# Kernel optimization log

Hardware: AMD Instinct MI355X
Metric: run time of the kernel (lower is better)

Reference implementation:

```python
import jax, jax.numpy as jnp
import numpy as np

N, C, EMB, OUT, HID, HEADS, K, R, E = 100000, 256, 256, 8, 256, 4, 20000, 16, 800000
RETR_IN = EMB + OUT + 1  # z_retr + o_retr + retr_score
DH = HID // HEADS


def _lin(key, fi, fo):
    return jax.random.normal(key, (fi, fo), jnp.float32) / np.sqrt(fi)


def setup_inputs() -> dict:
    key = jax.random.key(0)
    ks = jax.random.split(key, 32)
    inp = {
        "h_cone": jax.random.normal(ks[0], (N, C), jnp.float32),
        "z_retr": jax.random.normal(ks[1], (K, R, EMB), jnp.float32),
        "o_retr": jax.random.normal(ks[2], (K, R, OUT), jnp.float32),
        "retr_score": jax.random.uniform(ks[3], (K, R), jnp.float32),
        "teacher_yhat": jax.random.normal(ks[4], (N, OUT), jnp.float32),
        "outpin_nids": jax.random.randint(ks[5], (K,), 0, N, jnp.int32),
        "edge_index": jax.random.randint(ks[6], (2, E), 0, N, jnp.int32),
        # retr_proj: Linear(RETR_IN,HID) -> ReLU -> Linear(HID,HID)
        "rp_W1": _lin(ks[7], RETR_IN, HID), "rp_b1": jnp.zeros((HID,), jnp.float32),
        "rp_W2": _lin(ks[8], HID, HID),     "rp_b2": jnp.zeros((HID,), jnp.float32),
        # query_proj: Linear(C, HID)
        "qp_W": _lin(ks[9], C, HID), "qp_b": jnp.zeros((HID,), jnp.float32),
        # MultiheadAttention packed q/k/v projection + output projection
        "in_proj_W": _lin(ks[10], HID, 3 * HID), "in_proj_b": jnp.zeros((3 * HID,), jnp.float32),
        "out_proj_W": _lin(ks[11], HID, HID),    "out_proj_b": jnp.zeros((HID,), jnp.float32),
        # gate_net: Linear(C+HID,HID) -> ReLU -> Linear(HID,C) -> Sigmoid
        "gate_W1": _lin(ks[12], C + HID, HID), "gate_b1": jnp.zeros((HID,), jnp.float32),
        "gate_W2": _lin(ks[13], HID, C),       "gate_b2": jnp.zeros((C,), jnp.float32),
        # update_net: Linear(HID,C) -> ReLU -> Linear(C,C)
        "upd_W1": _lin(ks[14], HID, C), "upd_b1": jnp.zeros((C,), jnp.float32),
        "upd_W2": _lin(ks[15], C, C),   "upd_b2": jnp.zeros((C,), jnp.float32),
        # cone GNN (LocalGNN gcn, 2 layers): C->HID, HID->HID with sym-normalized aggregation
        "gnn_W1": _lin(ks[16], C, HID),   "gnn_b1": jnp.zeros((HID,), jnp.float32),
        "gnn_W2": _lin(ks[17], HID, HID), "gnn_b2": jnp.zeros((HID,), jnp.float32),
        # head: Linear(HID,HID) -> ReLU -> Linear(HID,OUT) (orig zero-init; random here for nontrivial grads)
        "head_W1": _lin(ks[18], HID, HID), "head_b1": jnp.zeros((HID,), jnp.float32),
        "head_W2": _lin(ks[19], HID, OUT) * 0.01, "head_b2": jnp.zeros((OUT,), jnp.float32),
    }
    return inp


def _forward(h_cone, z_retr, o_retr, retr_score, teacher_yhat, outpin_nids, edge_index,
             rp_W1, rp_b1, rp_W2, rp_b2, qp_W, qp_b, in_proj_W, in_proj_b,
             out_proj_W, out_proj_b, gate_W1, gate_b1, gate_W2, gate_b2,
             upd_W1, upd_b1, upd_W2, upd_b2, gnn_W1, gnn_b1, gnn_W2, gnn_b2,
             head_W1, head_b1, head_W2, head_b2):
    # ---- retrieval aggregation: per-outpin cross-attn over R neighbors ----
    kv_in = jnp.concatenate([z_retr, o_retr, retr_score[..., None]], axis=-1)  # [K,R,RETR_IN]
    kv = jax.nn.relu(kv_in @ rp_W1 + rp_b1) @ rp_W2 + rp_b2                    # [K,R,HID]
    hq = h_cone[outpin_nids]                                                   # [K,C] gather
    q = hq @ qp_W + qp_b                                                       # [K,HID]
    Wq, Wk, Wv = jnp.split(in_proj_W, 3, axis=1)
    bq, bk, bv = jnp.split(in_proj_b, 3)
    qh = (q @ Wq + bq).reshape(K, HEADS, DH)
    kh = (kv @ Wk + bk).reshape(K, R, HEADS, DH)
    vh = (kv @ Wv + bv).reshape(K, R, HEADS, DH)
    att = jax.nn.softmax(jnp.einsum('khd,krhd->khr', qh, kh) / np.sqrt(DH), axis=-1)
    ctx = jnp.einsum('khr,krhd->khd', att, vh).reshape(K, HID)
    retr_ctx = ctx @ out_proj_W + out_proj_b                                   # [K,HID]
    # ---- gated outpin fusion + scatter back ----
    gate = jax.nn.sigmoid(jax.nn.relu(jnp.concatenate([hq, retr_ctx], axis=-1) @ gate_W1 + gate_b1) @ gate_W2 + gate_b2)
    update = jax.nn.relu(retr_ctx @ upd_W1 + upd_b1) @ upd_W2 + upd_b2         # [K,C]
    h = h_cone.at[outpin_nids].set(hq + gate * update)                         # scatter
    # ---- cone GNN: 2-layer GCN with self loops, symmetric normalization ----
    loops = jnp.arange(N, dtype=edge_index.dtype)
    src = jnp.concatenate([edge_index[0], loops])
    dst = jnp.concatenate([edge_index[1], loops])
    deg = jax.ops.segment_sum(jnp.ones_like(src, jnp.float32), dst, num_segments=N)
    norm = (jax.lax.rsqrt(deg[src]) * jax.lax.rsqrt(deg[dst]))[:, None]
    x1 = h @ gnn_W1 + gnn_b1
    h1 = jax.nn.relu(jax.ops.segment_sum(x1[src] * norm, dst, num_segments=N))
    x2 = h1 @ gnn_W2 + gnn_b2
    h2 = jax.ops.segment_sum(x2[src] * norm, dst, num_segments=N)
    # ---- residual head ----
    delta = jax.nn.relu(h2 @ head_W1 + head_b1) @ head_W2 + head_b2
    return teacher_yhat + delta


def reference(h_cone, z_retr, o_retr, retr_score, teacher_yhat, outpin_nids, edge_index,
              rp_W1, rp_b1, rp_W2, rp_b2, qp_W, qp_b, in_proj_W, in_proj_b,
              out_proj_W, out_proj_b, gate_W1, gate_b1, gate_W2, gate_b2,
              upd_W1, upd_b1, upd_W2, upd_b2, gnn_W1, gnn_b1, gnn_W2, gnn_b2,
              head_W1, head_b1, head_W2, head_b2):
    return _forward(h_cone, z_retr, o_retr, retr_score, teacher_yhat, outpin_nids, edge_index,
                    rp_W1, rp_b1, rp_W2, rp_b2, qp_W, qp_b, in_proj_W, in_proj_b,
                    out_proj_W, out_proj_b, gate_W1, gate_b1, gate_W2, gate_b2,
                    upd_W1, upd_b1, upd_W2, upd_b2, gnn_W1, gnn_b1, gnn_W2, gnn_b2,
                    head_W1, head_b1, head_W2, head_b2)
```

## Files before the change

### kernel.cpp

```cpp
#include <hip/hip_runtime.h>
#include <cstdint>
#include <cstddef>

typedef unsigned short u16;

#define NN    100000
#define OUTD  8
#define KKP   20000
#define RR    16
#define EE    800000
#define KRR   (KKP*RR)
#define KP    20096
#define NP    100096

typedef __bf16 v8bf __attribute__((ext_vector_type(8)));
typedef float  v4f  __attribute__((ext_vector_type(4)));

__device__ __forceinline__ float b2f(u16 u) {
    union { uint32_t i; float f; } v; v.i = (uint32_t)u << 16; return v.f;
}
__device__ __forceinline__ u16 f2b(float f) {
    union { float f; uint32_t i; } v; v.f = f;
    uint32_t i = v.i;
    return (u16)((i + 0x7fffu + ((i >> 16) & 1u)) >> 16);
}
__device__ __forceinline__ uint32_t pk2(float a, float b) {
    return (uint32_t)f2b(a) | ((uint32_t)f2b(b) << 16);
}

#define GLDS(g, l) __builtin_amdgcn_global_load_lds(                         \
    (const __attribute__((address_space(1))) void*)(g),                      \
    (__attribute__((address_space(3))) void*)(l), 16, 0, 0)

#define WAITVL(n) asm volatile("s_waitcnt vmcnt(" #n ") lgkmcnt(0)" ::: "memory")
#define BAR() __builtin_amdgcn_s_barrier()

template <int EPI, int OMODE, int A32, int RETR>
__launch_bounds__(256)
__global__ void gemm_bf_k(const void* __restrict__ Av, int lda, int M, int Ka,
                          const u16* __restrict__ Wt,
                          const float* __restrict__ bias,
                          void* __restrict__ Cv, int ldc,
                          const float* __restrict__ o_ex,
                          const float* __restrict__ s_ex,
                          const float* __restrict__ Wex)
{
    constexpr int NBA = A32 ? 2 : 3;
    __shared__ u16 As[NBA * 128 * 32];
    __shared__ u16 Bs[3 * 128 * 32];
    const int row0 = blockIdx.x * 128;
    const int col0 = blockIdx.y * 128;
    const int t    = threadIdx.x;
    const int lane = t & 63;
    const int w    = t >> 6;
    const int wm   = w & 1, wn = w >> 1;

    const int idx0 = t, idx1 = t + 256;
    const u16* Ab = (const u16*)Av;
    const float* Af = (const float*)Av;
    const u16* Ag0 = Ab + (size_t)(row0 + (idx0 >> 2)) * lda + (idx0 & 3) * 8;
    const u16* Ag1 = Ab + (size_t)(row0 + (idx1 >> 2)) * lda + (idx1 & 3) * 8;
    const float* Af0 = Af + (size_t)(row0 + (idx0 >> 2)) * lda + (idx0 & 3) * 8;
    const float* Af1 = Af + (size_t)(row0 + (idx1 >> 2)) * lda + (idx1 & 3) * 8;
    const u16* Bg0 = Wt + (size_t)(col0 + (idx0 >> 2)) * Ka + (idx0 & 3) * 8;
    const u16* Bg1 = Wt + (size_t)(col0 + (idx1 >> 2)) * Ka + (idx1 & 3) * 8;
    const int s0 = idx0 * 8, s1 = idx1 * 8;

    auto stageB = [&](int bi, int kk) {
        u16* bp = Bs + bi * (128 * 32);
        GLDS(Bg0 + kk, bp + s0);
        GLDS(Bg1 + kk, bp + s1);
    };
    auto stageA = [&](int bi, int kk) {
        u16* ap = As + bi * (128 * 32);
        GLDS(Ag0 + kk, ap + s0);
        GLDS(Ag1 + kk, ap + s1);
    };

    float4 P0, P1, P2, P3, Q0, Q1, Q2, Q3;
    auto loadP = [&](int kk) {
        P0 = *(const float4*)(Af0 + kk);     P1 = *(const float4*)(Af0 + kk + 4);
        P2 = *(const float4*)(Af1 + kk);     P3 = *(const float4*)(Af1 + kk + 4);
    };
    auto loadQ = [&](int kk) {
        Q0 = *(const float4*)(Af0 + kk);     Q1 = *(const float4*)(Af0 + kk + 4);
        Q2 = *(const float4*)(Af1 + kk);     Q3 = *(const float4*)(Af1 + kk + 4);
    };
    auto writeP = [&](int bi) {
        u16* ap = As + bi * (128 * 32);
        uint4 u0, u1;
        u0.x = pk2(P0.x, P0.y); u0.y = pk2(P0.z, P0.w);
        u0.z = pk2(P1.x, P1.y); u0.w = pk2(P1.z, P1.w);
        u1.x = pk2(P2.x, P2.y); u1.y = pk2(P2.z, P2.w);
        u1.z = pk2(P3.x, P3.y); u1.w = pk2(P3.z, P3.w);
        *(uint4*)(ap + s0) = u0;
        *(uint4*)(ap + s1) = u1;
    };
    auto writeQ = [&](int bi) {
        u16* ap = As + bi * (128 * 32);
        uint4 u0, u1;
        u0.x = pk2(Q0.x, Q0.y); u0.y = pk2(Q0.z, Q0.w);
        u0.z = pk2(Q1.x, Q1.y); u0.w = pk2(Q1.z, Q1.w);
        u1.x = pk2(Q2.x, Q2.y); u1.y = pk2(Q2.z, Q2.w);
        u1.z = pk2(Q3.x, Q3.y); u1.w = pk2(Q3.z, Q3.w);
        *(uint4*)(ap + s0) = u0;
        *(uint4*)(ap + s1) = u1;
    };

    v4f acc[4][4];
#pragma unroll
    for (int mi = 0; mi < 4; mi++)
#pragma unroll
        for (int ni = 0; ni < 4; ni++) acc[mi][ni] = 0.f;

    const int fr = lane & 15;
    const int fq = (lane >> 4) * 8;
    const int nk = Ka >> 5;

    if (A32) {
        loadP(0);
        stageB(0, 0);
        if (nk > 1) {
            loadQ(32);
            stageB(1, 32);
        }
        writeP(0);
        if (nk > 1) { WAITVL(6); }
        else        { WAITVL(0); }
    } else {
        stageA(0, 0); stageB(0, 0);
        if (nk > 1) { stageA(1, 32); stageB(1, 32); WAITVL(4); }
        else        { WAITVL(0); }
    }
    BAR();

    int rb = 0, sb = 2;
    for (int tI = 0; tI < nk; ++tI) {
        const bool st = (tI + 2) < nk;
        const int kk2 = (tI + 2) << 5;
        if (st) {
            if (A32) {
                if (tI & 1) loadQ(kk2); else loadP(kk2);
                stageB(sb, kk2);
            } else {
                stageA(sb, kk2);
                stageB(sb, kk2);
            }
        }
        const u16* Ar = As + (A32 ? (tI & 1) : rb) * (128 * 32);
        const u16* Br = Bs + rb * (128 * 32);
        v8bf af[4], bv[4];
#pragma unroll
        for (int mi = 0; mi < 4; mi++)
            af[mi] = *(const v8bf*)&Ar[(wm * 64 + mi * 16 + fr) * 32 + fq];
#pragma unroll
        for (int ni = 0; ni < 4; ni++)
            bv[ni] = *(const v8bf*)&Br[(wn * 64 + ni * 16 + fr) * 32 + fq];
#pragma unroll
        for (int mi = 0; mi < 4; mi++)
#pragma unroll
            for (int ni = 0; ni < 4; ni++)
                acc[mi][ni] = __builtin_amdgcn_mfma_f32_16x16x32_bf16(
                    af[mi], bv[ni], acc[mi][ni], 0, 0, 0);

        if (tI + 1 < nk) {
            if (A32) {
                if (tI & 1) writeP((tI + 1) & 1); else writeQ((tI + 1) & 1);
            }
            if (st) { if (A32) { WAITVL(6); } else { WAITVL(4); } }
            else    { WAITVL(0); }
            BAR();
        }
        rb = (rb == 2) ? 0 : rb + 1;
        sb = (sb == 2) ? 0 : sb + 1;
    }

    const int crow = wm * 64 + (lane >> 4) * 4;
    const int ccol = wn * 64 + (lane & 15);
    float bias_v[4];
#pragma unroll
    for (int ni = 0; ni < 4; ni++) bias_v[ni] = bias[col0 + ccol + ni * 16];

    u16*   Cb = (u16*)Cv;
    float* Cf = (float*)Cv;
#pragma unroll
    for (int mi = 0; mi < 4; mi++) {
#pragma unroll
        for (int reg = 0; reg < 4; reg++) {
            int r = row0 + crow + mi * 16 + reg;
            if (r >= M) continue;
            float ov[8], sv;
            if (RETR) {
#pragma unroll
                for (int u = 0; u < 8; u++) ov[u] = o_ex[(size_t)r * 8 + u];
                sv = s_ex[r];
            }
#pragma unroll
            for (int ni = 0; ni < 4; ni++) {
                int c = col0 + ccol + ni * 16;
                float v = acc[mi][ni][reg] + bias_v[ni];
                if (RETR) {
                    float e = sv * Wex[8 * 256 + c];
#pragma unroll
                    for (int u = 0; u < 8; u++) e = fmaf(ov[u], Wex[u * 256 + c], e);
                    v += e;
                }
                if (EPI == 1) v = fmaxf(v, 0.f);
                if (EPI == 2) v = 1.f / (1.f + expf(-v));
                if (OMODE == 1) Cb[(size_t)r * ldc + c] = f2b(v);
                else            Cf[(size_t)r * ldc + c] = v;
            }
        }
    }
}

__global__ void wtpose_k(const float* __restrict__ W, int ld, int coloff,
                         int fi, int Kpad, u16* __restrict__ Wt)
{
    int g = blockIdx.x * 256 + threadIdx.x;
    if (g >= 256 * Kpad) return;
    int o = g / Kpad, i = g - o * Kpad;
    Wt[g] = f2b(i < fi ? W[(size_t)i * ld + coloff + o] : 0.f);
}

__global__ void wfuse_k(const float* __restrict__ A, const float* __restrict__ Binw,
                        int ldb, int off, const float* __restrict__ ba,
                        const float* __restrict__ bb,
                        u16* __restrict__ Wt_out, float* __restrict__ bias_out)
{
    __shared__ float As[256];
    __shared__ float bs[256];
    int i = blockIdx.x, j = threadIdx.x;
    As[j] = A[(size_t)i * 256 + j];
    bs[j] = ba[j];
    __syncthreads();
    float acc = 0.f, accb = 0.f;
    for (int m = 0; m < 256; m++) {
        float bv = Binw[(size_t)m * ldb + off + j];
        acc = fmaf(As[m], bv, acc);
        if (i == 0) accb = fmaf(bs[m], bv, accb);
    }
    Wt_out[(size_t)j * 256 + i] = f2b(acc);
    if (i == 0) bias_out[j] = bb[j] + accb;
}

__global__ void conv_f2b_k(const float* __restrict__ src, u16* __restrict__ dst, size_t n4)
{
    size_t g = (size_t)blockIdx.x * 256 + threadIdx.x;
    if (g >= n4) return;
    float4 v = ((const float4*)src)[g];
    ((ushort4*)dst)[g] = make_ushort4(f2b(v.x), f2b(v.y), f2b(v.z), f2b(v.w));
}

__global__ void gather_hq_k(const float* __restrict__ hc, const int* __restrict__ nids,
                            u16* __restrict__ acat)
{
    int t = threadIdx.x;
    int k = blockIdx.x * 4 + (t >> 6);
    int c = t & 63;
    if (k >= KKP) return;
    int nid = nids[k];
    float4 v = ((const float4*)hc)[(size_t)nid * 64 + c];
    *(ushort4*)&acat[(size_t)k * 512 + c * 4] =
        make_ushort4(f2b(v.x), f2b(v.y), f2b(v.z), f2b(v.w));
}

__launch_bounds__(256)
__global__ void att_fused_k(const u16* __restrict__ qh, const u16* __restrict__ khv,
                            u16* __restrict__ ctx)
{
    int k = blockIdx.x;
    int t = threadIdx.x;
    int lane = t & 63;
    float qv = b2f(qh[(size_t)k * 256 + t]);
    const u16* kp = khv + (size_t)k * (RR * 512) + t;
    const u16* vp = kp + 256;
    float myscore = -1e30f;
#pragma unroll
    for (int r = 0; r < RR; r++) {
        float p = qv * b2f(kp[r * 512]);
#pragma unroll
        for (int off = 1; off < 64; off <<= 1) p += __shfl_xor(p, off);
        if (lane == r) myscore = p * 0.125f;
    }
    float m = (lane < RR) ? myscore : -1e30f;
#pragma unroll
    for (int off = 1; off < 16; off <<= 1) m = fmaxf(m, __shfl_xor(m, off));
    float pe = (lane < RR) ? expf(myscore - m) : 0.f;
    float ssum = pe;
#pragma unroll
    for (int off = 1; off < 16; off <<= 1) ssum += __shfl_xor(ssum, off);
    float pn = pe / ssum;
    float acc = 0.f;
#pragma unroll
    for (int r = 0; r < RR; r++) {
        float ar = __shfl(pn, r);
        acc = fmaf(ar, b2f(vp[r * 512]), acc);
    }
    ctx[(size_t)k * 256 + t] = f2b(acc);
}

__global__ void winner_k(const int* __restrict__ nids, int* __restrict__ winner)
{
    int gid = blockIdx.x * 256 + threadIdx.x;
    if (gid < KKP) atomicMax(&winner[nids[gid]], gid);
}

__global__ void scatter_h_k(const int* __restrict__ nids, const int* __restrict__ winner,
                            const float* __restrict__ hc, const float* __restrict__ gate,
                            const float* __restrict__ upd, u16* __restrict__ hb)
{
    int t = threadIdx.x;
    int k = blockIdx.x * 4 + (t >> 6);
    int c = t & 63;
    if (k >= KKP) return;
    int nid = nids[k];
    if (winner[nid] != k) return;
    float4 hv = ((const float4*)hc)[(size_t)nid * 64 + c];
    float4 gv = ((const float4*)gate)[(size_t)k * 64 + c];
    float4 uv = ((const float4*)upd)[(size_t)k * 64 + c];
    *(ushort4*)&hb[(size_t)nid * 256 + c * 4] = make_ushort4(
        f2b(hv.x + gv.x * uv.x), f2b(hv.y + gv.y * uv.y),
        f2b(hv.z + gv.z * uv.z), f2b(hv.w + gv.w * uv.w));
}

__global__ void edge_count_k(const int* __restrict__ dst, int* __restrict__ cnt, int e)
{
    int gid = blockIdx.x * 256 + threadIdx.x;
    if (gid < e) atomicAdd(&cnt[dst[gid]], 1);
}

__global__ void isd_k(const int* __restrict__ cnt, float* __restrict__ isd, int n)
{
    int gid = blockIdx.x * 256 + threadIdx.x;
    if (gid < n) isd[gid] = rsqrtf((float)(cnt[gid] + 1));
}

#define SCANB 1024
__global__ void scan1_k(const int* __restrict__ in, int* __restrict__ out,
                        int* __restrict__ bsums, int n)
{
    __shared__ int s[SCANB];
    int tid = threadIdx.x;
    int gid = blockIdx.x * SCANB + tid;
    int v = (gid < n) ? in[gid] : 0;
    s[tid] = v;
    __syncthreads();
    for (int off = 1; off < SCANB; off <<= 1) {
        int add = (tid >= off) ? s[tid - off] : 0;
        __syncthreads();
        s[tid] += add;
        __syncthreads();
    }
    if (gid < n) out[gid] = s[tid] - v;
    if (tid == SCANB - 1) bsums[blockIdx.x] = s[tid];
}

__global__ void scan2_k(int* bsums, int nb)
{
    if (threadIdx.x == 0 && blockIdx.x == 0) {
        int run = 0;
        for (int i = 0; i < nb; i++) { int v = bsums[i]; bsums[i] = run; run += v; }
    }
}

__global__ void scan3_k(int* __restrict__ out, const int* __restrict__ bsums, int n, int total)
{
    int gid = blockIdx.x * SCANB + threadIdx.x;
    if (gid < n) out[gid] += bsums[blockIdx.x];
    if (gid == 0) out[n] = total;
}

__global__ void csr_scatter_k(const int* __restrict__ src, const int* __restrict__ dst,
                              const int* __restrict__ row_start, int* __restrict__ cursor,
                              const float* __restrict__ isd,
                              int* __restrict__ csr_src, float* __restrict__ csr_w, int e)
{
    int gid = blockIdx.x * 256 + threadIdx.x;
    if (gid < e) {
        int sP = src[gid], dP = dst[gid];
        int pos = row_start[dP] + atomicAdd(&cursor[dP], 1);
        csr_src[pos] = sP;
        csr_w[pos] = isd[sP] * isd[dP];
    }
}

template <int RELU>
__launch_bounds__(256)
__global__ void gnn_agg_k(const u16* __restrict__ x, const int* __restrict__ row_start,
                          const int* __restrict__ csr_src, const float* __restrict__ csr_w,
                          const float* __restrict__ isd, u16* __restrict__ outp)
{
    int node = blockIdx.x * 4 + (threadIdx.x >> 6);
    int lane = threadIdx.x & 63;
    if (node >= NN) return;
    float si = isd[node];
    float sii = si * si;
    ushort4 sv = ((const ushort4*)x)[(size_t)node * 64 + lane];
    float a0 = b2f(sv.x) * sii, a1 = b2f(sv.y) * sii;
    float a2 = b2f(sv.z) * sii, a3 = b2f(sv.w) * sii;
    int s0 = row_start[node], s1 = row_start[node + 1];
    for (int j = s0; j < s1; j++) {
        int sP = csr_src[j];
        float wv = csr_w[j];
        ushort4 v = ((const ushort4*)x)[(size_t)sP * 64 + lane];
        a0 = fmaf(b2f(v.x), wv, a0);
        a1 = fmaf(b2f(v.y), wv, a1);
        a2 = fmaf(b2f(v.z), wv, a2);
        a3 = fmaf(b2f(v.w), wv, a3);
    }
    if (RELU) {
        a0 = fmaxf(a0, 0.f); a1 = fmaxf(a1, 0.f);
        a2 = fmaxf(a2, 0.f); a3 = fmaxf(a3, 0.f);
    }
    ((ushort4*)outp)[(size_t)node * 64 + lane] =
        make_ushort4(f2b(a0), f2b(a1), f2b(a2), f2b(a3));
}

__launch_bounds__(256)
__global__ void head_out_k(const u16* __restrict__ thid, const float* __restrict__ W2,
                           const float* __restrict__ b2, const float* __restrict__ teacher,
                           float* __restrict__ outp, int n)
{
    __shared__ float ts[32][257];
    __shared__ float w2s[256 * 8];
    int t = threadIdx.x;
    int rbase = blockIdx.x * 32;
    for (int i = t; i < 2048; i += 256) w2s[i] = W2[i];
    for (int i = t; i < 32 * 256; i += 256) {
        int rr = i >> 8, cc = i & 255;
        int gr = rbase + rr;
        ts[rr][cc] = (gr < n) ? b2f(thid[(size_t)gr * 256 + cc]) : 0.f;
    }
    __syncthreads();
    int rr = t >> 3, cc = t & 7;
    int gr = rbase + rr;
    if (gr >= n) return;
    float acc = b2[cc];
    for (int kk = 0; kk < 256; kk++)
        acc = fmaf(ts[rr][kk], w2s[kk * 8 + cc], acc);
    outp[(size_t)gr * 8 + cc] = teacher[(size_t)gr * 8 + cc] + acc;
}

extern "C" void kernel_launch(void* const* d_in, const int* in_sizes, int n_in,
                              void* d_out, int out_size, void* d_ws, size_t ws_size,
                              hipStream_t stream)
{
    (void)in_sizes; (void)n_in; (void)out_size; (void)ws_size;
    const float* h_cone     = (const float*)d_in[0];
    const float* z_retr     = (const float*)d_in[1];
    const float* o_retr     = (const float*)d_in[2];
    const float* retr_score = (const float*)d_in[3];
    const float* teacher    = (const float*)d_in[4];
    const int*   nids       = (const int*)d_in[5];
    const int*   edge       = (const int*)d_in[6];
    const float* rp_W1 = (const float*)d_in[7];   const float* rp_b1 = (const float*)d_in[8];
    const float* rp_W2 = (const float*)d_in[9];   const float* rp_b2 = (const float*)d_in[10];
    const float* qp_W  = (const float*)d_in[11];  const float* qp_b  = (const float*)d_in[12];
    const float* inW   = (const float*)d_in[13];  const float* inB   = (const float*)d_in[14];
    const float* outW  = (const float*)d_in[15];  const float* outB  = (const float*)d_in[16];
    const float* gW1   = (const float*)d_in[17];  const float* gB1   = (const float*)d_in[18];
    const float* gW2   = (const float*)d_in[19];  const float* gB2   = (const float*)d_in[20];
    const float* uW1   = (const float*)d_in[21];  const float* uB1   = (const float*)d_in[22];
    const float* uW2   = (const float*)d_in[23];  const float* uB2   = (const float*)d_in[24];
    const float* gnW1  = (const float*)d_in[25];  const float* gnB1  = (const float*)d_in[26];
    const float* gnW2  = (const float*)d_in[27];  const float* gnB2  = (const float*)d_in[28];
    const float* hW1   = (const float*)d_in[29];  const float* hB1   = (const float*)d_in[30];
    const float* hW2   = (const float*)d_in[31];  const float* hB2   = (const float*)d_in[32];
    float* out = (float*)d_out;

    char* ws = (char*)d_ws;
    size_t off = 0;
    auto alloc = [&](size_t bytes) -> void* {
        void* p = ws + off;
        off = (off + bytes + 255) & ~(size_t)255;
        return p;
    };
    u16* hidden = (u16*)alloc((size_t)KRR * 256 * 2);
    u16* khv    = (u16*)alloc((size_t)KRR * 512 * 2);
    u16* qhb    = (u16*)alloc((size_t)KP * 256 * 2);
    u16* ctxb   = (u16*)alloc((size_t)KP * 256 * 2);
    u16* acat   = (u16*)alloc((size_t)KP * 512 * 2);
    u16* ghid   = (u16*)alloc((size_t)KP * 256 * 2);
    float* gate = (float*)alloc((size_t)KP * 256 * 4);
    u16* uhid   = (u16*)alloc((size_t)KP * 256 * 2);
    float* upd  = (float*)alloc((size_t)KP * 256 * 4);
    u16* wt_rp1 = (u16*)alloc(256 * 256 * 2);
    u16* wt_kv  = (u16*)alloc(512 * 256 * 2);
    u16* wt_qf  = (u16*)alloc(256 * 256 * 2);
    u16* wt_o   = (u16*)alloc(256 * 256 * 2);
    u16* wt_g1  = (u16*)alloc(256 * 512 * 2);
    u16* wt_g2  = (u16*)alloc(256 * 256 * 2);
    u16* wt_u1  = (u16*)alloc(256 * 256 * 2);
    u16* wt_u2  = (u16*)alloc(256 * 256 * 2);
    u16* wt_gn1 = (u16*)alloc(256 * 256 * 2);
    u16* wt_gn2 = (u16*)alloc(256 * 256 * 2);
    u16* wt_h1  = (u16*)alloc(256 * 256 * 2);
    float* bias_kv = (float*)alloc(512 * 4);
    float* bias_qf = (float*)alloc(256 * 4);
    int*   winner    = (int*)alloc(NN * 4);
    int*   cnt       = (int*)alloc(NN * 4);
    int*   cursor    = (int*)alloc(NN * 4);
    int*   row_start = (int*)alloc((NN + 1) * 4);
    int*   bsums     = (int*)alloc(1024 * 4);
    float* isd       = (float*)alloc(NN * 4);
    int*   csr_src   = (int*)alloc((size_t)EE * 4);
    float* csr_w     = (float*)alloc((size_t)EE * 4);

    const size_t NPE = (size_t)NP * 256;
    u16* gZ0 = hidden;
    u16* gZ1 = hidden + NPE;
    u16* gZ2 = hidden + 2 * NPE;

    const int* esrc = edge;
    const int* edst = edge + EE;

    auto wtp = [&](const float* W, int ld, int coloff, int fi, int Kpad, u16* Wt) {
        wtpose_k<<<(256 * Kpad + 255) / 256, 256, 0, stream>>>(W, ld, coloff, fi, Kpad, Wt);
    };

    hipMemsetAsync(cnt, 0, NN * 4, stream);
    hipMemsetAsync(cursor, 0, NN * 4, stream);
    edge_count_k<<<(EE + 255) / 256, 256, 0, stream>>>(edst, cnt, EE);
    isd_k<<<(NN + 255) / 256, 256, 0, stream>>>(cnt, isd, NN);
    int nb = (NN + SCANB - 1) / SCANB;
    scan1_k<<<nb, SCANB, 0, stream>>>(cnt, row_start, bsums, NN);
    scan2_k<<<1, 64, 0, stream>>>(bsums, nb);
    scan3_k<<<nb, SCANB, 0, stream>>>(row_start, bsums, NN, EE);
    csr_scatter_k<<<(EE + 255) / 256, 256, 0, stream>>>(esrc, edst, row_start, cursor, isd,
                                                        csr_src, csr_w, EE);

    wtp(rp_W1, 256, 0, 256, 256, wt_rp1);
    wfuse_k<<<256, 256, 0, stream>>>(rp_W2, inW, 768, 256, rp_b2, inB + 256, wt_kv, bias_kv);
    wfuse_k<<<256, 256, 0, stream>>>(rp_W2, inW, 768, 512, rp_b2, inB + 512,
                                     wt_kv + 256 * 256, bias_kv + 256);
    wfuse_k<<<256, 256, 0, stream>>>(qp_W, inW, 768, 0, qp_b, inB, wt_qf, bias_qf);
    wtp(outW, 256, 0, 256, 256, wt_o);
    wtp(gW1,  256, 0, 512, 512, wt_g1);
    wtp(gW2,  256, 0, 256, 256, wt_g2);
    wtp(uW1,  256, 0, 256, 256, wt_u1);
    wtp(uW2,  256, 0, 256, 256, wt_u2);
    wtp(gnW1, 256, 0, 256, 256, wt_gn1);
    wtp(gnW2, 256, 0, 256, 256, wt_gn2);
    wtp(hW1,  256, 0, 256, 256, wt_h1);
    gather_hq_k<<<(KKP + 3) / 4, 256, 0, stream>>>(h_cone, nids, acat);

    gemm_bf_k<1, 1, 1, 1><<<dim3(KRR / 128, 2), 256, 0, stream>>>(
        z_retr, 256, KRR, 256, wt_rp1, rp_b1, hidden, 256,
        o_retr, retr_score, rp_W1 + 256 * 256);
    gemm_bf_k<0, 1, 0, 0><<<dim3(KRR / 128, 4), 256, 0, stream>>>(
        hidden, 256, KRR, 256, wt_kv, bias_kv, khv, 512, nullptr, nullptr, nullptr);
    gemm_bf_k<0, 1, 0, 0><<<dim3((KKP + 127) / 128, 2), 256, 0, stream>>>(
        acat, 512, KKP, 256, wt_qf, bias_qf, qhb, 256, nullptr, nullptr, nullptr);

    att_fused_k<<<KKP, 256, 0, stream>>>(qhb, khv, ctxb);
    gemm_bf_k<0, 1, 0, 0><<<dim3((KKP + 127) / 128, 2), 256, 0, stream>>>(
        ctxb, 256, KKP, 256, wt_o, outB, acat + 256, 512, nullptr, nullptr, nullptr);

    gemm_bf_k<1, 1, 0, 0><<<dim3((KKP + 127) / 128, 2), 256, 0, stream>>>(
        acat, 512, KKP, 512, wt_g1, gB1, ghid, 256, nullptr, nullptr, nullptr);
    gemm_bf_k<2, 2, 0, 0><<<dim3((KKP + 127) / 128, 2), 256, 0, stream>>>(
        ghid, 256, KKP, 256, wt_g2, gB2, gate, 256, nullptr, nullptr, nullptr);
    gemm_bf_k<1, 1, 0, 0><<<dim3((KKP + 127) / 128, 2), 256, 0, stream>>>(
        acat + 256, 512, KKP, 256, wt_u1, uB1, uhid, 256, nullptr, nullptr, nullptr);
    gemm_bf_k<0, 2, 0, 0><<<dim3((KKP + 127) / 128, 2), 256, 0, stream>>>(
        uhid, 256, KKP, 256, wt_u2, uB2, upd, 256, nullptr, nullptr, nullptr);

    conv_f2b_k<<<(int)(((size_t)NN * 64 + 255) / 256), 256, 0, stream>>>(
        h_cone, gZ0, (size_t)NN * 64);
    hipMemsetAsync(winner, 0xFF, NN * 4, stream);
    winner_k<<<(KKP + 255) / 256, 256, 0, stream>>>(nids, winner);
    scatter_h_k<<<(KKP + 3) / 4, 256, 0, stream>>>(nids, winner, h_cone, gate, upd, gZ0);

    gemm_bf_k<0, 1, 0, 0><<<dim3((NN + 127) / 128, 2), 256, 0, stream>>>(
        gZ0, 256, NN, 256, wt_gn1, gnB1, gZ1, 256, nullptr, nullptr, nullptr);
    gnn_agg_k<1><<<(NN + 3) / 4, 256, 0, stream>>>(gZ1, row_start, csr_src, csr_w, isd, gZ2);
    gemm_bf_k<0, 1, 0, 0><<<dim3((NN + 127) / 128, 2), 256, 0, stream>>>(
        gZ2, 256, NN, 256, wt_gn2, gnB2, gZ0, 256, nullptr, nullptr, nullptr);
    gnn_agg_k<0><<<(NN + 3) / 4, 256, 0, stream>>>(gZ0, row_start, csr_src, csr_w, isd, gZ1);
    gemm_bf_k<1, 1, 0, 0><<<dim3((NN + 127) / 128, 2), 256, 0, stream>>>(
        gZ1, 256, NN, 256, wt_h1, hB1, gZ2, 256, nullptr, nullptr, nullptr);
    head_out_k<<<(NN + 31) / 32, 256, 0, stream>>>(gZ2, hW2, hB2, teacher, out, NN);
}
```

Before: 1.812 ms.

## Fuse retrieval MLP, attention scores and value projection into one kernel

Replaces the separate retr_proj GEMM, K/V GEMM, Q GEMM and attention kernel with a single per-128-row kernel. The hidden activations stay in shared memory and are never written to HBM. Attention scores use a precomputed per-query vector (Q times W_k folded per head), and V is projected on the fly and reduced with the softmax weights. This removes the large KRR x 512 khv buffer and its global-memory round-trips. In exchange the kernel is heavy: about 160KB of LDS with launch_bounds(256,1), so occupancy is low, and the precision of the key projection changes.

```diff
diff --git a/kernel.cpp b/kernel.cpp
--- a/kernel.cpp
+++ b/kernel.cpp
@@ -214,6 +214,238 @@
     }
 }
 
+__launch_bounds__(256, 1)
+__global__ void retrfuse_k(const float* __restrict__ Zf,
+                           const u16*  __restrict__ W1t,
+                           const float* __restrict__ b1,
+                           const float* __restrict__ o_ex,
+                           const float* __restrict__ s_ex,
+                           const u16*  __restrict__ wqk,
+                           const u16*  __restrict__ Wv,
+                           const float* __restrict__ bv2,
+                           u16* __restrict__ ctx)
+{
+    __shared__ __align__(16) u16 Az[128 * 256];
+    __shared__ __align__(16) u16 Ax[128 * 32];
+    __shared__ __align__(16) u16 Bp[2 * 128 * 32];
+    __shared__ __align__(16) u16 Hs[128 * 256];
+
+    float* attL = (float*)Bp;
+
+    const int bx = blockIdx.x;
+    const int row0 = bx * 128;
+    const int t = threadIdx.x, lane = t & 63, w = t >> 6;
+    const int wm = w & 1, wn = w >> 1;
+    const int fr = lane & 15, fq = (lane >> 4) * 8;
+    const int idx0 = t, idx1 = t + 256;
+
+    auto stageBt = [&](int tts) {
+        int p2 = (tts >= 9) ? 1 : 0;
+        int s2 = tts - p2 * 9;
+        const u16* g0 = W1t + (size_t)(p2 * 128 + (idx0 >> 2)) * 288 + (idx0 & 3) * 8 + s2 * 32;
+        const u16* g1 = W1t + (size_t)(p2 * 128 + (idx1 >> 2)) * 288 + (idx1 & 3) * 8 + s2 * 32;
+        u16* bp = Bp + (tts & 1) * (128 * 32);
+        GLDS(g0, bp + idx0 * 8);
+        GLDS(g1, bp + idx1 * 8);
+    };
+
+    {
+        const float* zb = Zf + (size_t)row0 * 256;
+        float4 pa[4], pb[4];
+#pragma unroll
+        for (int j = 0; j < 4; j++) {
+            int c = j * 256 + t, r = c >> 5, sl = c & 31;
+            const float* g = zb + (size_t)r * 256 + sl * 8;
+            pa[j] = *(const float4*)g;
+            pb[j] = *(const float4*)(g + 4);
+        }
+        stageBt(0);
+#pragma unroll
+        for (int j = 0; j < 16; j++) {
+            int c = j * 256 + t, r = c >> 5, sl = c & 31;
+            int jr = j & 3;
+            uint4 u;
+            u.x = pk2(pa[jr].x, pa[jr].y); u.y = pk2(pa[jr].z, pa[jr].w);
+            u.z = pk2(pb[jr].x, pb[jr].y); u.w = pk2(pb[jr].z, pb[jr].w);
+            *(uint4*)((char*)Az + (size_t)r * 512 + ((sl ^ (r & 7)) * 16)) = u;
+            int jn = j + 4;
+            if (jn < 16) {
+                int cn = jn * 256 + t, rn = cn >> 5, sn = cn & 31;
+                const float* gn = zb + (size_t)rn * 256 + sn * 8;
+                pa[jr] = *(const float4*)gn;
+                pb[jr] = *(const float4*)(gn + 4);
+            }
+        }
+#pragma unroll
+        for (int j = 0; j < 2; j++) {
+            int c = j * 256 + t, r = c >> 2, sl = c & 3;
+            int rg = row0 + r;
+            uint4 u = make_uint4(0u, 0u, 0u, 0u);
+            if (sl == 0) {
+                float4 o0 = *(const float4*)(o_ex + (size_t)rg * 8);
+                float4 o1 = *(const float4*)(o_ex + (size_t)rg * 8 + 4);
+                u.x = pk2(o0.x, o0.y); u.y = pk2(o0.z, o0.w);
+                u.z = pk2(o1.x, o1.y); u.w = pk2(o1.z, o1.w);
+            } else if (sl == 1) {
+                u.x = pk2(s_ex[rg], 0.f);
+            }
+            *(uint4*)((char*)Ax + r * 64 + ((sl ^ (r & 3)) * 16)) = u;
+        }
+        WAITVL(0);
+        BAR();
+    }
+
+    v4f acc[4][4];
+#pragma unroll
+    for (int mi = 0; mi < 4; mi++)
+#pragma unroll
+        for (int ni = 0; ni < 4; ni++) acc[mi][ni] = 0.f;
+
+    for (int tt = 0; tt < 18; ++tt) {
+        if (tt + 1 < 18) stageBt(tt + 1);
+        const int pass = (tt >= 9) ? 1 : 0;
+        const int s = tt - pass * 9;
+        const u16* Br = Bp + (tt & 1) * (128 * 32);
+        v8bf af[4], bb[4];
+#pragma unroll
+        for (int mi = 0; mi < 4; mi++) {
+            int row = wm * 64 + mi * 16 + fr;
+            if (s < 8)
+                af[mi] = *(const v8bf*)((const char*)Az + (size_t)row * 512 +
+                                        (((s * 4 + (fq >> 3)) ^ (row & 7)) * 16));
+            else
+                af[mi] = *(const v8bf*)((const char*)Ax + row * 64 +
+                                        (((fq >> 3) ^ (row & 3)) * 16));
+        }
+#pragma unroll
+        for (int ni = 0; ni < 4; ni++)
+            bb[ni] = *(const v8bf*)&Br[(wn * 64 + ni * 16 + fr) * 32 + fq];
+#pragma unroll
+        for (int mi = 0; mi < 4; mi++)
+#pragma unroll
+            for (int ni = 0; ni < 4; ni++)
+                acc[mi][ni] = __builtin_amdgcn_mfma_f32_16x16x32_bf16(
+                    af[mi], bb[ni], acc[mi][ni], 0, 0, 0);
+
+        if (s == 8) {
+            const int col0p = pass * 128;
+            const int crow = wm * 64 + (lane >> 4) * 4;
+            const int ccol = wn * 64 + fr;
+            float bvv[4];
+#pragma unroll
+            for (int ni = 0; ni < 4; ni++) bvv[ni] = b1[col0p + ccol + ni * 16];
+#pragma unroll
+            for (int mi = 0; mi < 4; mi++)
+#pragma unroll
+                for (int reg = 0; reg < 4; reg++) {
+                    int rl = crow + mi * 16 + reg;
+#pragma unroll
+                    for (int ni = 0; ni < 4; ni++) {
+                        int c = col0p + ccol + ni * 16;
+                        float v = fmaxf(acc[mi][ni][reg] + bvv[ni], 0.f);
+                        *(u16*)((char*)Hs + (size_t)rl * 512 +
+                                (((c >> 3) ^ (rl & 7)) * 16) + (c & 7) * 2) = f2b(v);
+                    }
+                }
+#pragma unroll
+            for (int mi = 0; mi < 4; mi++)
+#pragma unroll
+                for (int ni = 0; ni < 4; ni++) acc[mi][ni] = 0.f;
+        }
+        if (tt < 17) { WAITVL(0); BAR(); }
+    }
+
+    auto stageV = [&](int rr) {
+#pragma unroll
+        for (int j = 0; j < 4; j++) {
+            int c = j * 256 + t;
+            int tile = c >> 9, cc = c & 511;
+            int vr = cc >> 5, sp = cc & 31;
+            int nts = tile * 8 + rr;
+            const u16* g = Wv + (size_t)(nts * 16 + vr) * 256 + ((sp ^ (vr & 7)) * 8);
+            GLDS(g, (u16*)((char*)Az + 16384 + (tile * 2 + (rr & 1)) * 8192 + cc * 16));
+        }
+    };
+#pragma unroll
+    for (int j = 0; j < 4; j++) {
+        int c = j * 256 + t;
+        GLDS(wqk + (size_t)(bx * 8) * 1024 + c * 8, (u16*)((char*)Az + c * 16));
+    }
+    stageV(0);
+    WAITVL(4);
+    BAR();
+
+#pragma unroll
+    for (int kk = 0; kk < 2; kk++) {
+        int kloc = w * 2 + kk;
+        v4f sc; sc = 0.f;
+#pragma unroll
+        for (int s = 0; s < 8; s++) {
+            int row = kloc * 16 + fr;
+            v8bf ha = *(const v8bf*)((const char*)Hs + (size_t)row * 512 +
+                                     (((s * 4 + (fq >> 3)) ^ (row & 7)) * 16));
+            v4f zf; zf = 0.f;
+            v8bf bq = __builtin_bit_cast(v8bf, zf);
+            if (fr < 4)
+                bq = *(const v8bf*)((const char*)Az + kloc * 2048 + fr * 512 + s * 64 + fq * 2);
+            sc = __builtin_amdgcn_mfma_f32_16x16x32_bf16(ha, bq, sc, 0, 0, 0);
+        }
+        float s0 = sc[0] * 0.125f, s1 = sc[1] * 0.125f;
+        float s2 = sc[2] * 0.125f, s3 = sc[3] * 0.125f;
+        float mx = fmaxf(fmaxf(s0, s1), fmaxf(s2, s3));
+        mx = fmaxf(mx, __shfl_xor(mx, 16));
+        mx = fmaxf(mx, __shfl_xor(mx, 32));
+        float p0 = __expf(s0 - mx), p1 = __expf(s1 - mx);
+        float p2 = __expf(s2 - mx), p3 = __expf(s3 - mx);
+        float sm = p0 + p1 + p2 + p3;
+        sm += __shfl_xor(sm, 16);
+        sm += __shfl_xor(sm, 32);
+        float inv = 1.f / sm;
+        if (fr < 4) {
+            float4 a4 = make_float4(p0 * inv, p1 * inv, p2 * inv, p3 * inv);
+            *(float4*)&attL[kloc * 64 + fr * 16 + (lane >> 4) * 4] = a4;
+        }
+    }
+    WAITVL(0);
+    BAR();
+
+    const int khalf = w & 1, nth = w >> 1;
+    v8bf af4[4][8];
+#pragma unroll
+    for (int kj = 0; kj < 4; kj++) {
+        int row = (khalf * 4 + kj) * 16 + fr;
+#pragma unroll
+        for (int s = 0; s < 8; s++)
+            af4[kj][s] = *(const v8bf*)((const char*)Hs + (size_t)row * 512 +
+                                        (((s * 4 + (fq >> 3)) ^ (row & 7)) * 16));
+    }
+    for (int r = 0; r < 8; ++r) {
+        if (r < 7) stageV(r + 1);
+        int nt = nth * 8 + r;
+        const char* cb = (const char*)Az + 16384 + (nth * 2 + (r & 1)) * 8192;
+        v8bf bvf[8];
+#pragma unroll
+        for (int s = 0; s < 8; s++)
+            bvf[s] = *(const v8bf*)(cb + fr * 512 + (((s * 4 + (fq >> 3)) ^ (fr & 7)) * 16));
+        float bvb = bv2[nt * 16 + fr];
+#pragma unroll
+        for (int kj = 0; kj < 4; kj++) {
+            int kloc = khalf * 4 + kj;
+            v4f d; d = 0.f;
+#pragma unroll
+            for (int s = 0; s < 8; s++)
+                d = __builtin_amdgcn_mfma_f32_16x16x32_bf16(af4[kj][s], bvf[s], d, 0, 0, 0);
+            float4 av = *(const float4*)&attL[kloc * 64 + (nt >> 2) * 16 + (lane >> 4) * 4];
+            float val = av.x * d[0] + av.y * d[1] + av.z * d[2] + av.w * d[3];
+            val += __shfl_xor(val, 16);
+            val += __shfl_xor(val, 32);
+            if (lane < 16)
+                ctx[(size_t)(bx * 8 + kloc) * 256 + nt * 16 + lane] = f2b(val + bvb);
+        }
+        if (r < 7) { WAITVL(4); BAR(); }
+    }
+}
+
 __global__ void wtpose_k(const float* __restrict__ W, int ld, int coloff,
                          int fi, int Kpad, u16* __restrict__ Wt)
 {
@@ -226,7 +458,8 @@
 __global__ void wfuse_k(const float* __restrict__ A, const float* __restrict__ Binw,
                         int ldb, int off, const float* __restrict__ ba,
                         const float* __restrict__ bb,
-                        u16* __restrict__ Wt_out, float* __restrict__ bias_out)
+                        u16* __restrict__ Wt_out, float* __restrict__ bias_out,
+                        float* __restrict__ out32)
 {
     __shared__ float As[256];
     __shared__ float bs[256];
@@ -241,7 +474,33 @@
         if (i == 0) accb = fmaf(bs[m], bv, accb);
     }
     Wt_out[(size_t)j * 256 + i] = f2b(acc);
+    if (out32) out32[(size_t)j * 256 + i] = acc;
     if (i == 0) bias_out[j] = bb[j] + accb;
+}
+
+__global__ void qkfuse_k(const float* __restrict__ Qf32, const float* __restrict__ Wk32,
+                         const float* __restrict__ bqf,
+                         u16* __restrict__ Wtqk, float* __restrict__ bqk)
+{
+    __shared__ float wk[64];
+    __shared__ float bq[64];
+    int b = blockIdx.x;
+    int h = b >> 8, m = b & 255;
+    int c = threadIdx.x;
+    if (c < 64) {
+        wk[c] = Wk32[(size_t)(h * 64 + c) * 256 + m];
+        bq[c] = bqf[h * 64 + c];
+    }
+    __syncthreads();
+    float acc = 0.f;
+    for (int d = 0; d < 64; d++)
+        acc = fmaf(Qf32[(size_t)(h * 64 + d) * 256 + c], wk[d], acc);
+    Wtqk[(size_t)b * 256 + c] = f2b(acc);
+    if (c == 0) {
+        float ab = 0.f;
+        for (int d = 0; d < 64; d++) ab = fmaf(bq[d], wk[d], ab);
+        bqk[b] = ab;
+    }
 }
 
 __global__ void conv_f2b_k(const float* __restrict__ src, u16* __restrict__ dst, size_t n4)
@@ -263,41 +522,6 @@
     float4 v = ((const float4*)hc)[(size_t)nid * 64 + c];
     *(ushort4*)&acat[(size_t)k * 512 + c * 4] =
         make_ushort4(f2b(v.x), f2b(v.y), f2b(v.z), f2b(v.w));
-}
-
-__launch_bounds__(256)
-__global__ void att_fused_k(const u16* __restrict__ qh, const u16* __restrict__ khv,
-                            u16* __restrict__ ctx)
-{
-    int k = blockIdx.x;
-    int t = threadIdx.x;
-    int lane = t & 63;
-    float qv = b2f(qh[(size_t)k * 256 + t]);
-    const u16* kp = khv + (size_t)k * (RR * 512) + t;
-    const u16* vp = kp + 256;
-    float myscore = -1e30f;
-#pragma unroll
-    for (int r = 0; r < RR; r++) {
-        float p = qv * b2f(kp[r * 512]);
-#pragma unroll
-        for (int off = 1; off < 64; off <<= 1) p += __shfl_xor(p, off);
-        if (lane == r) myscore = p * 0.125f;
-    }
-    float m = (lane < RR) ? myscore : -1e30f;
-#pragma unroll
-    for (int off = 1; off < 16; off <<= 1) m = fmaxf(m, __shfl_xor(m, off));
-    float pe = (lane < RR) ? expf(myscore - m) : 0.f;
-    float ssum = pe;
-#pragma unroll
-    for (int off = 1; off < 16; off <<= 1) ssum += __shfl_xor(ssum, off);
-    float pn = pe / ssum;
-    float acc = 0.f;
-#pragma unroll
-    for (int r = 0; r < RR; r++) {
-        float ar = __shfl(pn, r);
-        acc = fmaf(ar, b2f(vp[r * 512]), acc);
-    }
-    ctx[(size_t)k * 256 + t] = f2b(acc);
 }
 
 __global__ void winner_k(const int* __restrict__ nids, int* __restrict__ winner)
@@ -477,15 +701,14 @@
         return p;
     };
     u16* hidden = (u16*)alloc((size_t)KRR * 256 * 2);
-    u16* khv    = (u16*)alloc((size_t)KRR * 512 * 2);
-    u16* qhb    = (u16*)alloc((size_t)KP * 256 * 2);
     u16* ctxb   = (u16*)alloc((size_t)KP * 256 * 2);
     u16* acat   = (u16*)alloc((size_t)KP * 512 * 2);
     u16* ghid   = (u16*)alloc((size_t)KP * 256 * 2);
     float* gate = (float*)alloc((size_t)KP * 256 * 4);
     u16* uhid   = (u16*)alloc((size_t)KP * 256 * 2);
     float* upd  = (float*)alloc((size_t)KP * 256 * 4);
-    u16* wt_rp1 = (u16*)alloc(256 * 256 * 2);
+    u16* wqk_g  = (u16*)alloc((size_t)KP * 1024 * 2);
+    u16* wt_rp1 = (u16*)alloc(256 * 288 * 2);
     u16* wt_kv  = (u16*)alloc(512 * 256 * 2);
     u16* wt_qf  = (u16*)alloc(256 * 256 * 2);
     u16* wt_o   = (u16*)alloc(256 * 256 * 2);
@@ -496,8 +719,12 @@
     u16* wt_gn1 = (u16*)alloc(256 * 256 * 2);
     u16* wt_gn2 = (u16*)alloc(256 * 256 * 2);
     u16* wt_h1  = (u16*)alloc(256 * 256 * 2);
+    u16* wt_qk  = (u16*)alloc(1024 * 256 * 2);
+    float* Qf32 = (float*)alloc(256 * 256 * 4);
+    float* Wk32 = (float*)alloc(256 * 256 * 4);
     float* bias_kv = (float*)alloc(512 * 4);
     float* bias_qf = (float*)alloc(256 * 4);
+    float* bias_qk = (float*)alloc(1024 * 4);
     int*   winner    = (int*)alloc(NN * 4);
     int*   cnt       = (int*)alloc(NN * 4);
     int*   cursor    = (int*)alloc(NN * 4);
@@ -530,11 +757,14 @@
     csr_scatter_k<<<(EE + 255) / 256, 256, 0, stream>>>(esrc, edst, row_start, cursor, isd,
                                                         csr_src, csr_w, EE);
 
-    wtp(rp_W1, 256, 0, 256, 256, wt_rp1);
-    wfuse_k<<<256, 256, 0, stream>>>(rp_W2, inW, 768, 256, rp_b2, inB + 256, wt_kv, bias_kv);
+    wtp(rp_W1, 256, 0, 265, 288, wt_rp1);
+    wfuse_k<<<256, 256, 0, stream>>>(rp_W2, inW, 768, 256, rp_b2, inB + 256,
+                                     wt_kv, bias_kv, Wk32);
     wfuse_k<<<256, 256, 0, stream>>>(rp_W2, inW, 768, 512, rp_b2, inB + 512,
-                                     wt_kv + 256 * 256, bias_kv + 256);
-    wfuse_k<<<256, 256, 0, stream>>>(qp_W, inW, 768, 0, qp_b, inB, wt_qf, bias_qf);
+                                     wt_kv + 256 * 256, bias_kv + 256, nullptr);
+    wfuse_k<<<256, 256, 0, stream>>>(qp_W, inW, 768, 0, qp_b, inB,
+                                     wt_qf, bias_qf, Qf32);
+    qkfuse_k<<<1024, 256, 0, stream>>>(Qf32, Wk32, bias_qf, wt_qk, bias_qk);
     wtp(outW, 256, 0, 256, 256, wt_o);
     wtp(gW1,  256, 0, 512, 512, wt_g1);
     wtp(gW2,  256, 0, 256, 256, wt_g2);
@@ -545,15 +775,13 @@
     wtp(hW1,  256, 0, 256, 256, wt_h1);
     gather_hq_k<<<(KKP + 3) / 4, 256, 0, stream>>>(h_cone, nids, acat);
 
-    gemm_bf_k<1, 1, 1, 1><<<dim3(KRR / 128, 2), 256, 0, stream>>>(
-        z_retr, 256, KRR, 256, wt_rp1, rp_b1, hidden, 256,
-        o_retr, retr_score, rp_W1 + 256 * 256);
-    gemm_bf_k<0, 1, 0, 0><<<dim3(KRR / 128, 4), 256, 0, stream>>>(
-        hidden, 256, KRR, 256, wt_kv, bias_kv, khv, 512, nullptr, nullptr, nullptr);
-    gemm_bf_k<0, 1, 0, 0><<<dim3((KKP + 127) / 128, 2), 256, 0, stream>>>(
-        acat, 512, KKP, 256, wt_qf, bias_qf, qhb, 256, nullptr, nullptr, nullptr);
-
-    att_fused_k<<<KKP, 256, 0, stream>>>(qhb, khv, ctxb);
+    gemm_bf_k<0, 1, 0, 0><<<dim3((KKP + 127) / 128, 8), 256, 0, stream>>>(
+        acat, 512, KKP, 256, wt_qk, bias_qk, wqk_g, 1024, nullptr, nullptr, nullptr);
+
+    retrfuse_k<<<KRR / 128, 256, 0, stream>>>(
+        z_retr, wt_rp1, rp_b1, o_retr, retr_score,
+        wqk_g, wt_kv + 256 * 256, bias_kv + 256, ctxb);
+
     gemm_bf_k<0, 1, 0, 0><<<dim3((KKP + 127) / 128, 2), 256, 0, stream>>>(
         ctxb, 256, KKP, 256, wt_o, outB, acat + 256, 512, nullptr, nullptr, nullptr);
 
```

Result: faster. 1.610 ms (-11.1%).
